# Kernel tuning notes

Hardware: AMD Instinct MI355X
Metric: run time of the kernel (lower is better)

The kernel has to match this reference:

```python
import jax, jax.numpy as jnp
import numpy as np

B, T, C, H = 4, 2048, 1024, 16
D = C // H  # head dim = 64


def setup_inputs() -> dict:
    key = jax.random.key(0)
    ks = jax.random.split(key, 8)
    s = 1.0 / np.sqrt(C)
    return {
        "x": jax.random.normal(ks[0], (B, T, C), jnp.float32),
        "mask": jax.random.randint(ks[1], (B, T), 0, 2, jnp.int32),
        "Wq": jax.random.normal(ks[2], (C, C), jnp.float32) * s,
        "bq": jnp.zeros((C,), jnp.float32),
        "Wk": jax.random.normal(ks[3], (C, C), jnp.float32) * s,
        "bk": jnp.zeros((C,), jnp.float32),
        "Wv": jax.random.normal(ks[4], (C, C), jnp.float32) * s,
        "bv": jnp.zeros((C,), jnp.float32),
    }


def reference(x, mask, Wq, bq, Wk, bk, Wv, bv):
    # QKV projections (nn.Linear: x @ W.T + b); W stored here as [out,in] -> use W.T
    q = x @ Wq.T + bq
    k = x @ Wk.T + bk
    v = x @ Wv.T + bv
    # split heads: [B,T,C] -> [B,H,T,D]
    q = q.reshape(B, T, H, D).transpose(0, 2, 1, 3)
    k = k.reshape(B, T, H, D).transpose(0, 2, 1, 3)
    v = v.reshape(B, T, H, D).transpose(0, 2, 1, 3)
    # scaled dot-product attention scores [B,H,T,T]
    attn = jnp.einsum("bhqd,bhkd->bhqk", q, k) / jnp.sqrt(jnp.float32(D))
    # additive mask over key positions: attn - inf*(1-mask), expressed stably
    big_neg = jnp.float32(-1e30)
    attn = jnp.where(mask[:, None, None, :] > 0, attn, big_neg)
    attn = jax.nn.softmax(attn, axis=-1)
    # dropout p=0 -> identity
    y = jnp.einsum("bhqk,bhkd->bhqd", attn, v)
    # merge heads: [B,H,T,D] -> [B,T,C]
    return y.transpose(0, 2, 1, 3).reshape(B, T, C)
```

## Files before the change

### kernel.cpp

```cpp
#include <hip/hip_runtime.h>
#include <stdint.h>

#define BB 4
#define TT 2048
#define CC 1024
#define HH 16
#define DD 64
#define MM (BB * TT)

typedef unsigned short u16;
typedef unsigned int   u32;
typedef __attribute__((ext_vector_type(8))) short short8;
typedef _Float16 half8  __attribute__((ext_vector_type(8)));
typedef __fp16   fp16x2 __attribute__((ext_vector_type(2)));
typedef __attribute__((ext_vector_type(4))) float f32x4;
typedef __attribute__((ext_vector_type(4))) unsigned short u16x4;
typedef __attribute__((ext_vector_type(4))) unsigned int u32x4;

#if __has_builtin(__builtin_amdgcn_exp2f)
#define EXP2(x) __builtin_amdgcn_exp2f(x)
#else
#define EXP2(x) __expf(0.69314718055994531f * (x))
#endif

__device__ inline u16 f2bf(float f) {
    union { float f; unsigned u; } v; v.f = f;
    unsigned r = 0x7fffu + ((v.u >> 16) & 1u);
    return (u16)((v.u + r) >> 16);
}
__device__ inline u16 f2h(float f) {
    union { _Float16 h; u16 u; } c; c.h = (_Float16)f; return c.u;
}
__device__ inline u32 pkh(float a, float b) {
    union { fp16x2 h; u32 u; } c;
    c.h = __builtin_amdgcn_cvt_pkrtz(a, b);
    return c.u;
}
__device__ inline u32 pkmask(int a, int b) {
    return ((u32)(-a) & 0xFFFFu) | ((u32)(-b) << 16);
}

#define NX (MM * CC / 4)
#define NW (CC * CC / 4)
#define NPM (BB * 1024)
__global__ void cvt_all(const float* __restrict__ x,  const float* __restrict__ Wq,
                        const float* __restrict__ Wk, const float* __restrict__ Wv,
                        const int* __restrict__ mask,
                        u16* __restrict__ xb, u16* __restrict__ Wb,
                        u32* __restrict__ pm) {
    int i = blockIdx.x * blockDim.x + threadIdx.x;
    if (i >= NX + 3 * NW) {
        int idx = i - (NX + 3 * NW);
        if (idx < NPM) {
            int b = idx >> 10, r = idx & 1023;
            int kt = r >> 5, lq = (r >> 3) & 3, j = r & 7;
            int key = kt * 64 + (j >> 2) * 32 + ((j >> 1) & 1) * 16 + lq * 4 + (j & 1) * 2;
            pm[idx] = pkmask(mask[b * TT + key], mask[b * TT + key + 1]);
        }
        return;
    }
    const float* src; u16* dst; int j;
    if (i < NX)               { src = x;  dst = xb;                       j = i; }
    else if (i < NX + NW)     { src = Wq; dst = Wb;                       j = i - NX; }
    else if (i < NX + 2 * NW) { src = Wk; dst = Wb + (size_t)CC * CC;     j = i - NX - NW; }
    else                      { src = Wv; dst = Wb + (size_t)2 * CC * CC; j = i - NX - 2 * NW; }
    float4 v = ((const float4*)src)[j];
    u16x4 o;
    o.x = f2bf(v.x); o.y = f2bf(v.y); o.z = f2bf(v.z); o.w = f2bf(v.w);
    ((u16x4*)dst)[j] = o;
}

__global__ void qkv_gemm(const u16* __restrict__ xb, const u16* __restrict__ Wb,
                         const float* __restrict__ bq, const float* __restrict__ bk,
                         const float* __restrict__ bv,
                         u16* __restrict__ Qh, u16* __restrict__ Kh, u16* __restrict__ Vt)
{
    const int f0  = blockIdx.x + 8 * (blockIdx.y + 64 * blockIdx.z);
    const int xcd = f0 & 7, g = f0 >> 3;
    const int mi  = g & 7, n_ = (g >> 3) & 7;
    const int z   = g >> 6;
    const int m0  = (xcd * 8 + mi) * 128, n0 = n_ * 128;

    const u16* W = Wb + (size_t)z * CC * CC;
    const float* bias = (z == 0) ? bq : ((z == 1) ? bk : bv);
    const float scale = (z == 0) ? 0.18033688011112042f : 1.0f;

    __shared__ __align__(16) u16 As[128][32];
    __shared__ __align__(16) u16 Bs[128][32];

    const int tid = threadIdx.x;
    const int l  = tid & 63, w = tid >> 6;
    const int wm = w >> 1,  wn = w & 1;
    const int lr = l & 15,  lq = l >> 4;

    f32x4 acc[4][4] = {};

    const u16* aLDS = (z == 2) ? &As[0][0] : &Bs[0][0];
    const u16* bLDS = (z == 2) ? &Bs[0][0] : &As[0][0];

    for (int kt = 0; kt < CC; kt += 32) {
        __syncthreads();
        #pragma unroll
        for (int r = 0; r < 2; ++r) {
            int c   = (r * 4 + w) * 64 + l;
            int row = c >> 2, kc = c & 3;
            const u16* ga = xb + (size_t)(m0 + row) * CC + kt + kc * 8;
            __builtin_amdgcn_global_load_lds(
                (const __attribute__((address_space(1))) void*)ga,
                (__attribute__((address_space(3))) void*)(&As[0][0] + (size_t)c * 8), 16, 0, 0);
            const u16* gb = W + (size_t)(n0 + row) * CC + kt + kc * 8;
            __builtin_amdgcn_global_load_lds(
                (const __attribute__((address_space(1))) void*)gb,
                (__attribute__((address_space(3))) void*)(&Bs[0][0] + (size_t)c * 8), 16, 0, 0);
        }
        __syncthreads();

        short8 af[4], bfr[4];
        #pragma unroll
        for (int mi2 = 0; mi2 < 4; ++mi2)
            af[mi2] = *(const short8*)(aLDS + (size_t)(wm * 64 + mi2 * 16 + lr) * 32 + lq * 8);
        #pragma unroll
        for (int ni = 0; ni < 4; ++ni)
            bfr[ni] = *(const short8*)(bLDS + (size_t)(wn * 64 + ni * 16 + lr) * 32 + lq * 8);
        #pragma unroll
        for (int mi2 = 0; mi2 < 4; ++mi2)
            #pragma unroll
            for (int ni = 0; ni < 4; ++ni)
                acc[mi2][ni] = __builtin_amdgcn_mfma_f32_16x16x32_bf16(
                    af[mi2], bfr[ni], acc[mi2][ni], 0, 0, 0);
    }

    if (z == 2) {
        #pragma unroll
        for (int ni = 0; ni < 4; ++ni) {
            int n = n0 + wn * 64 + ni * 16 + lr;
            float bvv = bias[n];
            int h = n >> 6, d = n & 63;
            #pragma unroll
            for (int mi2 = 0; mi2 < 4; ++mi2) {
                int mbase = m0 + wm * 64 + mi2 * 16 + lq * 4;
                int b = mbase >> 11, t0 = mbase & (TT - 1);
                int gk  = (t0 >> 2) & 7;
                int t0p = (t0 & ~31) | (((gk & 3) << 3) | ((gk >> 2) << 2));
                u16x4 pkv;
                #pragma unroll
                for (int r = 0; r < 4; ++r)
                    pkv[r] = f2h(acc[mi2][ni][r] + bvv);
                *(u16x4*)&Vt[((size_t)(b * HH + h) * DD + d) * TT + t0p] = pkv;
            }
        }
    } else {
        u16* out = (z == 0) ? Qh : Kh;
        #pragma unroll
        for (int mi2 = 0; mi2 < 4; ++mi2) {
            int nb = n0 + wm * 64 + mi2 * 16 + lq * 4;
            float4 b4 = *(const float4*)&bias[nb];
            int h = nb >> 6, d0 = nb & 63;
            #pragma unroll
            for (int ni = 0; ni < 4; ++ni) {
                int m = m0 + wn * 64 + ni * 16 + lr;
                int b = m >> 11, t = m & (TT - 1);
                u16x4 pkv;
                pkv.x = f2h((acc[mi2][ni][0] + b4.x) * scale);
                pkv.y = f2h((acc[mi2][ni][1] + b4.y) * scale);
                pkv.z = f2h((acc[mi2][ni][2] + b4.z) * scale);
                pkv.w = f2h((acc[mi2][ni][3] + b4.w) * scale);
                *(u16x4*)&out[((size_t)(b * HH + h) * TT + t) * DD + d0] = pkv;
            }
        }
    }
}

__global__ __launch_bounds__(256, 4)
void attn_kernel(const u16* __restrict__ Qh, const u16* __restrict__ Kh,
                 const u16* __restrict__ Vt, const u32* __restrict__ pm,
                 float* __restrict__ out)
{
    const int f   = blockIdx.x + (TT / 128) * (blockIdx.y + HH * blockIdx.z);
    const int xcd = f & 7, g = f >> 3;
    const int bh  = xcd * 8 + (g >> 4);
    const int qt  = g & 15;
    const int b   = bh >> 4, h = bh & 15;

    const int tid = threadIdx.x;
    const int l  = tid & 63, w = tid >> 6;
    const int lr = l & 15,  lq = l >> 4;

    __shared__ __align__(16) u16 Ks[2][64][72];
    __shared__ __align__(16) u16 Vs[2][2][64][40];

    const size_t base = (size_t)(b * HH + h) * TT * DD;
    const int q0 = qt * 128 + w * 32;

    half8 qf[2][2];
    #pragma unroll
    for (int qg = 0; qg < 2; ++qg)
        #pragma unroll
        for (int c = 0; c < 2; ++c)
            qf[qg][c] = *(const half8*)(Qh + base + (size_t)(q0 + qg * 16 + lr) * DD
                                        + c * 32 + lq * 8);

    const int kk = tid >> 3, dc = tid & 7;
    u16* k_dst0 = &Ks[0][kk][dc * 8];
    const u16* k_base = Kh + base + (size_t)kk * DD + dc * 8;
    const int vd = tid >> 2, vck = tid & 3;
    u16* v_dst0 = &Vs[0][0][vd][vck * 8];
    const u16* v_base = Vt + base + (size_t)vd * TT + vck * 8;
    const u32* pm_base = pm + b * 1024 + lq * 8;

    const int VHALF = 64 * 40;
    const int VBUF  = 2 * VHALF;
    const int KHALF = 32 * 72;
    const int KBUF  = 64 * 72;

    union { u32 u[4]; half8 h; } one_u;
    one_u.u[0] = one_u.u[1] = one_u.u[2] = one_u.u[3] = 0x3C003C00u;
    const half8 ones = one_u.h;

    {
        half8 k0 = *(const half8*)k_base;
        half8 k1 = *(const half8*)(k_base + 32 * DD);
        half8 v0 = *(const half8*)v_base;
        half8 v1 = *(const half8*)(v_base + 32);
        *(half8*)k_dst0 = k0;
        *(half8*)(k_dst0 + KHALF) = k1;
        *(half8*)v_dst0 = v0;
        *(half8*)(v_dst0 + VHALF) = v1;
    }

    f32x4 o[2][5] = {};

    const int NT = TT / 64;
    __syncthreads();

    for (int kt = 0; kt < NT; ++kt) {
        const int p = kt & 1;
        int ktn = (kt + 1 < NT) ? kt + 1 : NT - 1;
        const u16* kp = k_base + (size_t)ktn * 64 * DD;
        half8 kreg0 = *(const half8*)kp;
        half8 kreg1 = *(const half8*)(kp + 32 * DD);
        const u16* vp = v_base + ktn * 64;
        half8 vreg0 = *(const half8*)vp;
        half8 vreg1 = *(const half8*)(vp + 32);
        u32x4 am0 = *(const u32x4*)(pm_base + kt * 32);
        u32x4 am1 = *(const u32x4*)(pm_base + kt * 32 + 4);

        half8 kf[4][2];
        #pragma unroll
        for (int kg = 0; kg < 4; ++kg)
            #pragma unroll
            for (int c = 0; c < 2; ++c)
                kf[kg][c] = *(const half8*)&Ks[p][kg * 16 + lr][c * 32 + lq * 8];

        f32x4 s[4][2];
        #pragma unroll
        for (int kg = 0; kg < 4; ++kg)
            #pragma unroll
            for (int qg = 0; qg < 2; ++qg) {
                f32x4 zz = {};
                zz = __builtin_amdgcn_mfma_f32_16x16x32_f16(kf[kg][0], qf[qg][0], zz, 0, 0, 0);
                zz = __builtin_amdgcn_mfma_f32_16x16x32_f16(kf[kg][1], qf[qg][1], zz, 0, 0, 0);
                s[kg][qg] = zz;
            }

        half8 pf[2][2];
        #pragma unroll
        for (int hf = 0; hf < 2; ++hf) {
            const u32x4 am = hf ? am1 : am0;
            #pragma unroll
            for (int qg = 0; qg < 2; ++qg) {
                u32x4 pk;
                pk[0] = pkh(EXP2(s[2*hf][qg][0]),   EXP2(s[2*hf][qg][1]))   & am[0];
                pk[1] = pkh(EXP2(s[2*hf][qg][2]),   EXP2(s[2*hf][qg][3]))   & am[1];
                pk[2] = pkh(EXP2(s[2*hf+1][qg][0]), EXP2(s[2*hf+1][qg][1])) & am[2];
                pk[3] = pkh(EXP2(s[2*hf+1][qg][2]), EXP2(s[2*hf+1][qg][3])) & am[3];
                pf[hf][qg] = (half8&)pk;
            }
        }

        #pragma unroll
        for (int hf = 0; hf < 2; ++hf) {
            #pragma unroll
            for (int dg = 0; dg < 4; ++dg) {
                half8 vf = *(const half8*)&Vs[p][hf][dg * 16 + lr][lq * 8];
                #pragma unroll
                for (int qg = 0; qg < 2; ++qg)
                    o[qg][dg] = __builtin_amdgcn_mfma_f32_16x16x32_f16(pf[hf][qg], vf, o[qg][dg], 0, 0, 0);
            }
            #pragma unroll
            for (int qg = 0; qg < 2; ++qg)
                o[qg][4] = __builtin_amdgcn_mfma_f32_16x16x32_f16(pf[hf][qg], ones, o[qg][4], 0, 0, 0);
        }

        u16* kd = k_dst0 + (p ^ 1) * KBUF;
        *(half8*)kd = kreg0;
        *(half8*)(kd + KHALF) = kreg1;
        u16* vdst = v_dst0 + (p ^ 1) * VBUF;
        *(half8*)vdst = vreg0;
        *(half8*)(vdst + VHALF) = vreg1;
        __syncthreads();
    }

    #pragma unroll
    for (int qg = 0; qg < 2; ++qg)
        #pragma unroll
        for (int r = 0; r < 4; ++r) {
            float inv = 1.f / o[qg][4][r];
            int t = q0 + qg * 16 + lq * 4 + r;
            float* op = out + (size_t)(b * TT + t) * CC + h * DD;
            #pragma unroll
            for (int dg = 0; dg < 4; ++dg)
                op[dg * 16 + lr] = o[qg][dg][r] * inv;
        }
}

extern "C" void kernel_launch(void* const* d_in, const int* in_sizes, int n_in,
                              void* d_out, int out_size, void* d_ws, size_t ws_size,
                              hipStream_t stream) {
    const float* x    = (const float*)d_in[0];
    const int*   mask = (const int*)d_in[1];
    const float* Wq   = (const float*)d_in[2];
    const float* bq   = (const float*)d_in[3];
    const float* Wk   = (const float*)d_in[4];
    const float* bk   = (const float*)d_in[5];
    const float* Wv   = (const float*)d_in[6];
    const float* bv   = (const float*)d_in[7];
    float* out = (float*)d_out;

    u16* xb = (u16*)d_ws;
    u16* Wb = xb + (size_t)MM * CC;
    u16* Qh = Wb + (size_t)3 * CC * CC;
    u16* Kh = Qh + (size_t)MM * CC;
    u16* Vt = Kh + (size_t)MM * CC;
    u32* pm = (u32*)(Vt + (size_t)MM * CC);

    {
        int total = NX + 3 * NW + NPM;
        cvt_all<<<(total + 255) / 256, 256, 0, stream>>>(x, Wq, Wk, Wv, mask, xb, Wb, pm);
    }

    qkv_gemm<<<dim3(8, 64, 3), 256, 0, stream>>>(xb, Wb, bq, bk, bv, Qh, Kh, Vt);

    attn_kernel<<<dim3(TT / 128, HH, BB), 256, 0, stream>>>(Qh, Kh, Vt, pm, out);
}
```

Measured before the change: 239.5 us.

## Software-pipeline PV matmul one tile behind QK and exp in attention loop

Restructures the attention loop so the P·V MFMAs for the previous key tile run at the start of the next iteration, interleaved with the QK^T and exp work of the current tile. The goal is to overlap the exp/pack VALU work with matrix instructions. A third buffer is not used, so an extra __syncthreads is added before overwriting the other LDS buffer. Launch bounds drop from 4 to 2 blocks per SM to give room for the extra live P registers, which may lower occupancy.

```diff
diff --git a/kernel.cpp b/kernel.cpp
--- a/kernel.cpp
+++ b/kernel.cpp
@@ -171,7 +171,7 @@
     }
 }
 
-__global__ __launch_bounds__(256, 4)
+__global__ __launch_bounds__(256, 2)
 void attn_kernel(const u16* __restrict__ Qh, const u16* __restrict__ Kh,
                  const u16* __restrict__ Vt, const u32* __restrict__ pm,
                  float* __restrict__ out)
@@ -229,12 +229,36 @@
     }
 
     f32x4 o[2][5] = {};
+    half8 pfp[2][2];
 
     const int NT = TT / 64;
     __syncthreads();
 
+#define PV_BLOCK(vb)                                                            \
+    {                                                                           \
+        _Pragma("unroll")                                                       \
+        for (int hf = 0; hf < 2; ++hf) {                                        \
+            _Pragma("unroll")                                                   \
+            for (int dg = 0; dg < 4; ++dg) {                                    \
+                half8 vf = *(const half8*)&Vs[vb][hf][dg * 16 + lr][lq * 8];    \
+                _Pragma("unroll")                                               \
+                for (int qg = 0; qg < 2; ++qg)                                  \
+                    o[qg][dg] = __builtin_amdgcn_mfma_f32_16x16x32_f16(         \
+                        pfp[hf][qg], vf, o[qg][dg], 0, 0, 0);                   \
+            }                                                                   \
+            _Pragma("unroll")                                                   \
+            for (int qg = 0; qg < 2; ++qg)                                      \
+                o[qg][4] = __builtin_amdgcn_mfma_f32_16x16x32_f16(              \
+                    pfp[hf][qg], ones, o[qg][4], 0, 0, 0);                      \
+        }                                                                       \
+    }
+
     for (int kt = 0; kt < NT; ++kt) {
         const int p = kt & 1;
+
+        if (kt > 0)
+            PV_BLOCK(p ^ 1)
+
         int ktn = (kt + 1 < NT) ? kt + 1 : NT - 1;
         const u16* kp = k_base + (size_t)ktn * 64 * DD;
         half8 kreg0 = *(const half8*)kp;
@@ -263,7 +287,6 @@
                 s[kg][qg] = zz;
             }
 
-        half8 pf[2][2];
         #pragma unroll
         for (int hf = 0; hf < 2; ++hf) {
             const u32x4 am = hf ? am1 : am0;
@@ -274,23 +297,11 @@
                 pk[1] = pkh(EXP2(s[2*hf][qg][2]),   EXP2(s[2*hf][qg][3]))   & am[1];
                 pk[2] = pkh(EXP2(s[2*hf+1][qg][0]), EXP2(s[2*hf+1][qg][1])) & am[2];
                 pk[3] = pkh(EXP2(s[2*hf+1][qg][2]), EXP2(s[2*hf+1][qg][3])) & am[3];
-                pf[hf][qg] = (half8&)pk;
+                pfp[hf][qg] = (half8&)pk;
             }
         }
 
-        #pragma unroll
-        for (int hf = 0; hf < 2; ++hf) {
-            #pragma unroll
-            for (int dg = 0; dg < 4; ++dg) {
-                half8 vf = *(const half8*)&Vs[p][hf][dg * 16 + lr][lq * 8];
-                #pragma unroll
-                for (int qg = 0; qg < 2; ++qg)
-                    o[qg][dg] = __builtin_amdgcn_mfma_f32_16x16x32_f16(pf[hf][qg], vf, o[qg][dg], 0, 0, 0);
-            }
-            #pragma unroll
-            for (int qg = 0; qg < 2; ++qg)
-                o[qg][4] = __builtin_amdgcn_mfma_f32_16x16x32_f16(pf[hf][qg], ones, o[qg][4], 0, 0, 0);
-        }
+        __syncthreads();
 
         u16* kd = k_dst0 + (p ^ 1) * KBUF;
         *(half8*)kd = kreg0;
@@ -300,6 +311,9 @@
         *(half8*)(vdst + VHALF) = vreg1;
         __syncthreads();
     }
+
+    PV_BLOCK((NT - 1) & 1)
+#undef PV_BLOCK
 
     #pragma unroll
     for (int qg = 0; qg < 2; ++qg)
```

Measured after the change: 240.9 us. Within noise of the previous version (+0.6%).
